# Performance work log

Hardware: AMD Instinct MI355X
Metric: run time of the kernel (lower is better)

The kernel has to match this reference:

```python
import jax, jax.numpy as jnp
import numpy as np

E = 512      # embed_size
H = 8        # heads
HD = E // H  # head_dim
TN = 288     # time_num
FE = 4       # forward_expansion
N, T = 64, 512


def layernorm(x, g, b, eps=1e-5):
    mu = jnp.mean(x, axis=-1, keepdims=True)
    var = jnp.mean((x - mu) ** 2, axis=-1, keepdims=True)
    return (x - mu) * jax.lax.rsqrt(var + eps) * g + b


def setup_inputs() -> dict:
    key = jax.random.key(0)
    ks = jax.random.split(key, 12)
    w = lambda k, sh: jax.random.normal(k, sh, dtype=jnp.float32) * 0.02
    return {
        "value": jax.random.normal(ks[0], (N, T, E), dtype=jnp.float32),
        "key_in": jax.random.normal(ks[1], (N, T, E), dtype=jnp.float32),
        "query": jax.random.normal(ks[2], (N, T, E), dtype=jnp.float32),
        "i": 37,
        # One_hot_encoder params: learned identity-init table + linear to embed
        "I_mat": jnp.eye(TN, dtype=jnp.float32),
        "oh_W": w(ks[3], (TN, E)), "oh_b": jnp.zeros((E,), jnp.float32),
        # per-head projections (shared across heads, as in the torch module)
        "Wv": w(ks[4], (HD, HD)), "Wk": w(ks[5], (HD, HD)), "Wq": w(ks[6], (HD, HD)),
        "Wo": w(ks[7], (E, E)), "bo": jnp.zeros((E,), jnp.float32),
        "g1": jnp.ones((E,), jnp.float32), "b1": jnp.zeros((E,), jnp.float32),
        "g2": jnp.ones((E,), jnp.float32), "b2": jnp.zeros((E,), jnp.float32),
        "W1": w(ks[8], (E, FE * E)), "bf1": jnp.zeros((FE * E,), jnp.float32),
        "W2": w(ks[9], (FE * E, E)), "bf2": jnp.zeros((E,), jnp.float32),
    }


def reference(value, key_in, query, i, I_mat, oh_W, oh_b, Wv, Wk, Wq, Wo, bo,
              g1, b1, g2, b2, W1, bf1, W2, bf2):
    n, t, c = query.shape
    # One_hot_encoder: rows i..i+T-1 (mod time_num) of learned table -> linear
    rows = (i + jnp.arange(t)) % TN
    onehot = I_mat[rows] @ oh_W + oh_b            # (T, E), broadcast over N
    q_in = query + onehot[None, :, :]
    # per-head projections
    v = value.reshape(n, t, H, HD) @ Wv           # (N,T,H,HD)
    k = key_in.reshape(n, t, H, HD) @ Wk
    qh = q_in.reshape(n, t, H, HD) @ Wq
    # attention (note: scale uses sqrt(embed_size), per original code)
    energy = jnp.einsum("nqhd,nkhd->nhqk", qh, k) / jnp.sqrt(jnp.float32(E))
    attn = jax.nn.softmax(energy, axis=-1)
    out = jnp.einsum("nhqk,nkhd->nqhd", attn, v).reshape(n, t, E)
    out = out @ Wo + bo
    # residual + LN + FFN + residual + LN (dropout=0 -> identity)
    x = layernorm(out + q_in, g1, b1)
    ff = jax.nn.relu(x @ W1 + bf1) @ W2 + bf2
    return layernorm(ff + x, g2, b2)
```

## Files before the change

### kernel.cpp

```cpp
#include <hip/hip_runtime.h>

typedef __attribute__((ext_vector_type(8))) short s16x8;
typedef __attribute__((ext_vector_type(4))) float f32x4;

#define TN 288

__device__ __forceinline__ unsigned short f2bf(float f) {
  union { float f; unsigned u; } v; v.f = f;
  unsigned r = v.u + 0x7fffu + ((v.u >> 16) & 1u);
  return (unsigned short)(r >> 16);
}
__device__ __forceinline__ float bf2f(unsigned short u) {
  union { float f; unsigned u; } v; v.u = ((unsigned)u) << 16;
  return v.f;
}
__device__ __forceinline__ unsigned lds_addr(const void* p) {
  return (unsigned)(unsigned long long)(const __attribute__((address_space(3))) char*)p;
}
__device__ __forceinline__ void async_copy16(unsigned short* lds, const unsigned short* g) {
  __builtin_amdgcn_global_load_lds(
      (const __attribute__((address_space(1))) unsigned int*)g,
      (__attribute__((address_space(3))) unsigned int*)lds, 16, 0, 0);
}

__device__ __forceinline__ void pack_body(const float* __restrict__ W,
    unsigned short* __restrict__ out, int N, long t) {
  int lr = (int)(t & 15);
  int lg = (int)((t >> 4) & 3);
  long g6 = t >> 6;
  int nt = N >> 4;
  int n16 = (int)(g6 % nt);
  int kb = (int)(g6 / nt) << 5;
  int k = kb + lg * 8;
  int col = n16 * 16 + lr;
  s16x8 v;
#pragma unroll
  for (int j = 0; j < 8; ++j) v[j] = (short)f2bf(W[(size_t)(k + j) * N + col]);
  *(s16x8*)(out + t * 8) = v;
}

__global__ __launch_bounds__(256) void prep_kernel(const int* __restrict__ pi,
    const float* __restrict__ I_mat, const float* __restrict__ ohW,
    const float* __restrict__ ohb, float* __restrict__ onehot,
    const float* __restrict__ Wv, const float* __restrict__ Wk,
    const float* __restrict__ Wq, unsigned short* __restrict__ Wv_b,
    unsigned short* __restrict__ Wk_b, unsigned short* __restrict__ Wq_b,
    const float* __restrict__ Wo, const float* __restrict__ W1,
    const float* __restrict__ W2, unsigned short* __restrict__ Wop,
    unsigned short* __restrict__ W1p, unsigned short* __restrict__ W2p) {
  int b = blockIdx.x, tid = threadIdx.x;
  if (b < 512) {
    int t = b;
    int r = (pi[0] + t) % TN;
    float acc0 = ohb[tid], acc1 = ohb[tid + 256];
    const float* Ir = I_mat + (size_t)r * TN;
    for (int j = 0; j < TN; ++j) {
      float iv = Ir[j];
      acc0 += iv * ohW[(size_t)j * 512 + tid];
      acc1 += iv * ohW[(size_t)j * 512 + tid + 256];
    }
    onehot[(size_t)t * 512 + tid] = acc0;
    onehot[(size_t)t * 512 + tid + 256] = acc1;
  } else if (b < 640) {
    pack_body(Wo, Wop, 512, (long)(b - 512) * 256 + tid);
  } else if (b < 1152) {
    pack_body(W1, W1p, 2048, (long)(b - 640) * 256 + tid);
  } else if (b < 1664) {
    pack_body(W2, W2p, 512, (long)(b - 1152) * 256 + tid);
  } else {
    int which = b - 1664;
    const float* src = which == 0 ? Wv : (which == 1 ? Wk : Wq);
    unsigned short* dst = which == 0 ? Wv_b : (which == 1 ? Wk_b : Wq_b);
    float sc = which == 2 ? 0.06375871424f : 1.f;
#pragma unroll
    for (int j = 0; j < 4; ++j) {
      int i = tid * 16 + j * 4;
      float4 f = *(const float4*)(src + i);
      unsigned lo = (unsigned)f2bf(f.x * sc) | ((unsigned)f2bf(f.y * sc) << 16);
      unsigned hi = (unsigned)f2bf(f.z * sc) | ((unsigned)f2bf(f.w * sc) << 16);
      *(uint2*)(dst + i) = make_uint2(lo, hi);
    }
  }
}

template<bool QIN, int OUTMODE>
__global__ __launch_bounds__(256) void proj_gemm(const float* __restrict__ A,
    const unsigned short* __restrict__ B, const float* __restrict__ onehot,
    unsigned short* __restrict__ C, int M, int N, int K) {
  __shared__ unsigned short As[64][40];
  __shared__ unsigned short Bs[64][40];
  __shared__ unsigned short Cs[64][72];
  const int m0 = blockIdx.x * 64, n0 = blockIdx.y * 64;
  const int tid = threadIdx.x, w = tid >> 6, l = tid & 63, lr = l & 15, lg = l >> 4;
  const int wr = (w >> 1) * 32, wc = (w & 1) * 32;
  const int aRow = (tid * 8) >> 5, aK = (tid * 8) & 31;
  const int bK = (tid * 8) >> 6, bCol = (tid * 8) & 63;
  f32x4 acc[2][2] = {};
  for (int kb = 0; kb < K; kb += 32) {
    size_t fl = (size_t)(m0 + aRow) * K + kb + aK;
    float4 f0 = *(const float4*)(A + fl);
    float4 f1 = *(const float4*)(A + fl + 4);
    if (QIN) {
      const float* oh = onehot + (fl & 262143);
      float4 o0 = *(const float4*)(oh);
      float4 o1 = *(const float4*)(oh + 4);
      f0.x += o0.x; f0.y += o0.y; f0.z += o0.z; f0.w += o0.w;
      f1.x += o1.x; f1.y += o1.y; f1.z += o1.z; f1.w += o1.w;
    }
    s16x8 av;
    av[0] = (short)f2bf(f0.x); av[1] = (short)f2bf(f0.y);
    av[2] = (short)f2bf(f0.z); av[3] = (short)f2bf(f0.w);
    av[4] = (short)f2bf(f1.x); av[5] = (short)f2bf(f1.y);
    av[6] = (short)f2bf(f1.z); av[7] = (short)f2bf(f1.w);
    *(s16x8*)&As[aRow][aK] = av;
    s16x8 bv = *(const s16x8*)(B + (size_t)(kb + bK) * N + n0 + bCol);
#pragma unroll
    for (int j = 0; j < 8; ++j) Bs[bCol + j][bK] = (unsigned short)bv[j];
    __syncthreads();
    s16x8 af0 = *(const s16x8*)&As[wr + lr][lg * 8];
    s16x8 af1 = *(const s16x8*)&As[wr + 16 + lr][lg * 8];
    s16x8 bf0 = *(const s16x8*)&Bs[wc + lr][lg * 8];
    s16x8 bf1 = *(const s16x8*)&Bs[wc + 16 + lr][lg * 8];
    acc[0][0] = __builtin_amdgcn_mfma_f32_16x16x32_bf16(af0, bf0, acc[0][0], 0, 0, 0);
    acc[0][1] = __builtin_amdgcn_mfma_f32_16x16x32_bf16(af0, bf1, acc[0][1], 0, 0, 0);
    acc[1][0] = __builtin_amdgcn_mfma_f32_16x16x32_bf16(af1, bf0, acc[1][0], 0, 0, 0);
    acc[1][1] = __builtin_amdgcn_mfma_f32_16x16x32_bf16(af1, bf1, acc[1][1], 0, 0, 0);
    __syncthreads();
  }
  if (OUTMODE == 0) {
#pragma unroll
    for (int fi = 0; fi < 2; ++fi)
#pragma unroll
      for (int fj = 0; fj < 2; ++fj)
#pragma unroll
        for (int r = 0; r < 4; ++r) {
          int row = m0 + wr + fi * 16 + lg * 4 + r;
          int col = n0 + wc + fj * 16 + lr;
          C[(size_t)row * N + col] = f2bf(acc[fi][fj][r]);
        }
  } else {
#pragma unroll
    for (int fi = 0; fi < 2; ++fi)
#pragma unroll
      for (int fj = 0; fj < 2; ++fj)
#pragma unroll
        for (int r = 0; r < 4; ++r)
          Cs[wr + fi * 16 + lg * 4 + r][wc + fj * 16 + lr] = f2bf(acc[fi][fj][r]);
    __syncthreads();
    int nIdx = m0 >> 12, t0 = (m0 >> 3) & 511;
#pragma unroll
    for (int it = 0; it < 2; ++it) {
      int p = tid + it * 256;
      int hh = p >> 6, d = p & 63;
      s16x8 vv;
#pragma unroll
      for (int j = 0; j < 8; ++j) vv[j] = (short)Cs[j * 8 + hh][d];
      *(s16x8*)(C + (((size_t)(nIdx * 8 + hh) * 64 + d) << 9) + t0) = vv;
    }
  }
}

template<bool RELU, bool OUTBF>
__global__ __launch_bounds__(256) void gemmF(
    const unsigned short* __restrict__ A, int lda,
    const unsigned short* __restrict__ Bp, int ldbp, int nOff,
    const float* __restrict__ bias, void* __restrict__ Cout, int ldc,
    int M, int K, int nby) {
  __shared__ unsigned short As[2][8192];
  const int tid = threadIdx.x, w = tid >> 6, l = tid & 63, lr = l & 15, lg = l >> 4;
  const int nwg = gridDim.x;
  const int bid = (blockIdx.x & 7) * (nwg >> 3) + (blockIdx.x >> 3);
  const int bx = bid / nby, by = bid % nby;
  const int m0 = bx * 128;
  const int wr = (w >> 1) * 64, wc = (w & 1) * 64;
  const int srow = tid >> 3, sc8 = tid & 7;
  const int gcol = (sc8 ^ (srow & 7)) * 8;
  const unsigned short* Ag = A + (size_t)(m0 + srow) * lda + gcol;
  const size_t ldaa = (size_t)32 * lda;
  const unsigned short* Bg = Bp +
      ((size_t)(nOff >> 4) + by * 8 + (wc >> 4)) * 512 + lg * 128 + lr * 8;
  const size_t bks = (size_t)ldbp * 512;

  f32x4 acc[4][4] = {};
  s16x8 b0[4], b1[4];

#pragma unroll
  for (int it = 0; it < 4; ++it)
    async_copy16(&As[0][(it * 256 + tid) * 8], Ag + it * ldaa);
#pragma unroll
  for (int fj = 0; fj < 4; ++fj) {
    b0[fj] = *(const s16x8*)(Bg + fj * 512);
    b1[fj] = *(const s16x8*)(Bg + bks + fj * 512);
  }
  __syncthreads();

  int buf = 0;
  for (int kb = 0; kb < K; kb += 64) {
    int kn = (kb + 64 < K) ? kb + 64 : 0;
#pragma unroll
    for (int it = 0; it < 4; ++it)
      async_copy16(&As[buf ^ 1][(it * 256 + tid) * 8], Ag + kn + it * ldaa);
    s16x8 b0n[4];
    {
      const unsigned short* p = Bg + ((size_t)(kn >> 5)) * bks;
#pragma unroll
      for (int fj = 0; fj < 4; ++fj) b0n[fj] = *(const s16x8*)(p + fj * 512);
    }
    {
      s16x8 af[4];
#pragma unroll
      for (int fi = 0; fi < 4; ++fi) {
        int row = wr + fi * 16 + lr;
        af[fi] = *(const s16x8*)&As[buf][row * 64 + ((lg ^ (row & 7)) * 8)];
      }
#pragma unroll
      for (int fi = 0; fi < 4; ++fi)
#pragma unroll
        for (int fj = 0; fj < 4; ++fj)
          acc[fi][fj] = __builtin_amdgcn_mfma_f32_16x16x32_bf16(af[fi], b0[fj], acc[fi][fj], 0, 0, 0);
    }
    s16x8 b1n[4];
    {
      const unsigned short* p = Bg + ((size_t)((kn + 32) >> 5)) * bks;
#pragma unroll
      for (int fj = 0; fj < 4; ++fj) b1n[fj] = *(const s16x8*)(p + fj * 512);
    }
    {
      s16x8 af[4];
#pragma unroll
      for (int fi = 0; fi < 4; ++fi) {
        int row = wr + fi * 16 + lr;
        af[fi] = *(const s16x8*)&As[buf][row * 64 + (((4 + lg) ^ (row & 7)) * 8)];
      }
#pragma unroll
      for (int fi = 0; fi < 4; ++fi)
#pragma unroll
        for (int fj = 0; fj < 4; ++fj)
          acc[fi][fj] = __builtin_amdgcn_mfma_f32_16x16x32_bf16(af[fi], b1[fj], acc[fi][fj], 0, 0, 0);
    }
    __syncthreads();
#pragma unroll
    for (int fj = 0; fj < 4; ++fj) { b0[fj] = b0n[fj]; b1[fj] = b1n[fj]; }
    buf ^= 1;
  }

#pragma unroll
  for (int fj = 0; fj < 4; ++fj) {
    int colL = by * 128 + wc + fj * 16 + lr;
    float bv = bias[nOff + colL];
#pragma unroll
    for (int fi = 0; fi < 4; ++fi)
#pragma unroll
      for (int r = 0; r < 4; ++r) {
        int row = m0 + wr + fi * 16 + lg * 4 + r;
        size_t ci = (size_t)row * ldc + colL;
        float v = acc[fi][fj][r] + bv;
        if (RELU) v = fmaxf(v, 0.f);
        if (OUTBF) ((unsigned short*)Cout)[ci] = f2bf(v);
        else ((float*)Cout)[ci] = v;
      }
  }
}

__global__ __launch_bounds__(256, 2) void attn_kernel(
    const unsigned short* __restrict__ Qp, const unsigned short* __restrict__ Kp,
    const unsigned short* __restrict__ Vt, unsigned short* __restrict__ Out) {
  __shared__ unsigned short KS[2][8192];
  __shared__ unsigned short P[4][16][132];
  const int bid = blockIdx.x;
  const int qh = bid >> 9, g = bid & 511, h = g & 7, n = g >> 3;
  const int tid = threadIdx.x, w = tid >> 6, l = tid & 63, lr = l & 15, lg = l >> 4;
  const int q0 = qh * 256;

  s16x8 qf[4][2];
#pragma unroll
  for (int rt = 0; rt < 4; ++rt) {
    const size_t qb = (((size_t)(n * 512 + q0 + w * 64 + rt * 16 + lr)) * 8 + h) * 64;
    qf[rt][0] = *(const s16x8*)(Qp + qb + lg * 8);
    qf[rt][1] = *(const s16x8*)(Qp + qb + 32 + lg * 8);
  }
  const unsigned short* Vb = Vt + ((size_t)(n * 8 + h)) * 32768 + (size_t)lr * 512 + lg * 8;

  const int krr = tid >> 3, kc8 = tid & 7;
  const int kcol = (kc8 ^ (krr & 7)) * 8;

  f32x4 oacc[4][4] = {};
  float m[4][4], lsum[4][4];
#pragma unroll
  for (int rt = 0; rt < 4; ++rt)
#pragma unroll
    for (int r = 0; r < 4; ++r) { m[rt][r] = -1e30f; lsum[rt][r] = 0.f; }
  s16x8 vreg[16];

#pragma unroll
  for (int it = 0; it < 4; ++it)
    async_copy16(&KS[0][(it * 256 + tid) * 8],
                 Kp + (((size_t)(n * 512 + it * 32 + krr)) * 8 + h) * 64 + kcol);
  __syncthreads();

#pragma unroll
  for (int c = 0; c < 4; ++c) {
    const int buf = c & 1;
    if (c < 3) {
#pragma unroll
      for (int it = 0; it < 4; ++it)
        async_copy16(&KS[buf ^ 1][(it * 256 + tid) * 8],
                     Kp + (((size_t)(n * 512 + (c + 1) * 128 + it * 32 + krr)) * 8 + h) * 64 + kcol);
    }
#pragma unroll
    for (int ks = 0; ks < 4; ++ks)
#pragma unroll
      for (int fj = 0; fj < 4; ++fj)
        vreg[ks * 4 + fj] = *(const s16x8*)(Vb + fj * 8192 + c * 128 + ks * 32);

#pragma unroll
    for (int rt = 0; rt < 4; ++rt) {
      f32x4 sacc[8];
      __builtin_amdgcn_s_setprio(1);
#pragma unroll
      for (int f = 0; f < 8; ++f) {
        int row = f * 16 + lr;
        s16x8 bk0 = *(const s16x8*)&KS[buf][row * 64 + ((lg ^ (row & 7)) * 8)];
        s16x8 bk1 = *(const s16x8*)&KS[buf][row * 64 + (((4 + lg) ^ (row & 7)) * 8)];
        f32x4 a = {};
        a = __builtin_amdgcn_mfma_f32_16x16x32_bf16(qf[rt][0], bk0, a, 0, 0, 0);
        a = __builtin_amdgcn_mfma_f32_16x16x32_bf16(qf[rt][1], bk1, a, 0, 0, 0);
        sacc[f] = a;
      }
      __builtin_amdgcn_s_setprio(0);

      float fs[4];
#pragma unroll
      for (int r = 0; r < 4; ++r) {
        float cm = sacc[0][r];
#pragma unroll
        for (int f = 1; f < 8; ++f) cm = fmaxf(cm, sacc[f][r]);
#pragma unroll
        for (int mk = 1; mk < 16; mk <<= 1) cm = fmaxf(cm, __shfl_xor(cm, mk));
        float mn = fmaxf(m[rt][r], cm);
        fs[r] = __builtin_amdgcn_exp2f(m[rt][r] - mn);
        m[rt][r] = mn;
        unsigned pa = lds_addr(&P[w][lg * 4 + r][lr]);
        float cs = 0.f;
#pragma unroll
        for (int f = 0; f < 8; ++f) {
          float p = __builtin_amdgcn_exp2f(sacc[f][r] - mn);
          asm volatile("ds_write_b16_d16_hi %0, %1 offset:%2"
                       :: "v"(pa), "v"(p), "i"(f * 32) : "memory");
          cs += p;
        }
#pragma unroll
        for (int mk = 1; mk < 16; mk <<= 1) cs += __shfl_xor(cs, mk);
        lsum[rt][r] = lsum[rt][r] * fs[r] + cs;
      }
#pragma unroll
      for (int fj = 0; fj < 4; ++fj)
#pragma unroll
        for (int r = 0; r < 4; ++r) oacc[rt][fj][r] *= fs[r];

      asm volatile("s_waitcnt lgkmcnt(0)" ::: "memory");
      __builtin_amdgcn_sched_barrier(0);
      __builtin_amdgcn_s_setprio(1);
#pragma unroll
      for (int ks = 0; ks < 4; ++ks) {
        s16x8 pa = *(const s16x8*)&P[w][lr][ks * 32 + lg * 8];
#pragma unroll
        for (int fj = 0; fj < 4; ++fj)
          oacc[rt][fj] = __builtin_amdgcn_mfma_f32_16x16x32_bf16(pa, vreg[ks * 4 + fj], oacc[rt][fj], 0, 0, 0);
      }
      __builtin_amdgcn_s_setprio(0);
    }
    __syncthreads();
  }

#pragma unroll
  for (int rt = 0; rt < 4; ++rt)
#pragma unroll
    for (int fj = 0; fj < 4; ++fj)
#pragma unroll
      for (int r = 0; r < 4; ++r) {
        int qrow = q0 + w * 64 + rt * 16 + lg * 4 + r;
        Out[((size_t)(n * 512 + qrow)) * 512 + h * 64 + fj * 16 + lr] =
            f2bf(oacc[rt][fj][r] / lsum[rt][r]);
      }
}

template<bool XBF, bool RBF, bool QIN, bool OUTBF>
__global__ __launch_bounds__(256) void ln_kernel(const void* __restrict__ Xv,
    const void* __restrict__ Rv, const float* __restrict__ onehot,
    const float* __restrict__ g, const float* __restrict__ bb,
    void* __restrict__ outv) {
  int row = blockIdx.x * 4 + (threadIdx.x >> 6);
  int l = threadIdx.x & 63;
  size_t base = (size_t)row * 512 + l * 8;
  float v[8];
  if (XBF) {
    s16x8 xv = *(const s16x8*)((const unsigned short*)Xv + base);
#pragma unroll
    for (int j = 0; j < 8; ++j) v[j] = bf2f((unsigned short)xv[j]);
  } else {
    const float* X = (const float*)Xv;
    float4 x0 = *(const float4*)(X + base);
    float4 x1 = *(const float4*)(X + base + 4);
    v[0] = x0.x; v[1] = x0.y; v[2] = x0.z; v[3] = x0.w;
    v[4] = x1.x; v[5] = x1.y; v[6] = x1.z; v[7] = x1.w;
  }
  if (RBF) {
    s16x8 rv = *(const s16x8*)((const unsigned short*)Rv + base);
#pragma unroll
    for (int j = 0; j < 8; ++j) v[j] += bf2f((unsigned short)rv[j]);
  } else {
    const float* R = (const float*)Rv;
    float4 r0 = *(const float4*)(R + base);
    float4 r1 = *(const float4*)(R + base + 4);
    v[0] += r0.x; v[1] += r0.y; v[2] += r0.z; v[3] += r0.w;
    v[4] += r1.x; v[5] += r1.y; v[6] += r1.z; v[7] += r1.w;
  }
  if (QIN) {
    size_t ob = (size_t)(row & 511) * 512 + l * 8;
    float4 o0 = *(const float4*)(onehot + ob);
    float4 o1 = *(const float4*)(onehot + ob + 4);
    v[0] += o0.x; v[1] += o0.y; v[2] += o0.z; v[3] += o0.w;
    v[4] += o1.x; v[5] += o1.y; v[6] += o1.z; v[7] += o1.w;
  }
  float s = 0.f, ss = 0.f;
#pragma unroll
  for (int j = 0; j < 8; ++j) { s += v[j]; ss += v[j] * v[j]; }
#pragma unroll
  for (int mk = 1; mk < 64; mk <<= 1) { s += __shfl_xor(s, mk); ss += __shfl_xor(ss, mk); }
  float mu = s * (1.f / 512.f);
  float inv = rsqrtf(ss * (1.f / 512.f) - mu * mu + 1e-5f);
#pragma unroll
  for (int j = 0; j < 8; ++j) {
    int e = l * 8 + j;
    float y = (v[j] - mu) * inv * g[e] + bb[e];
    if (OUTBF) ((unsigned short*)outv)[base + j] = f2bf(y);
    else ((float*)outv)[base + j] = y;
  }
}

extern "C" void kernel_launch(void* const* d_in, const int* in_sizes, int n_in,
                              void* d_out, int out_size, void* d_ws, size_t ws_size,
                              hipStream_t stream) {
  const float* value  = (const float*)d_in[0];
  const float* key_in = (const float*)d_in[1];
  const float* query  = (const float*)d_in[2];
  const int*   pi     = (const int*)d_in[3];
  const float* I_mat  = (const float*)d_in[4];
  const float* ohW    = (const float*)d_in[5];
  const float* ohb    = (const float*)d_in[6];
  const float* Wv     = (const float*)d_in[7];
  const float* Wk     = (const float*)d_in[8];
  const float* Wq     = (const float*)d_in[9];
  const float* Wo     = (const float*)d_in[10];
  const float* bo     = (const float*)d_in[11];
  const float* g1     = (const float*)d_in[12];
  const float* b1     = (const float*)d_in[13];
  const float* g2     = (const float*)d_in[14];
  const float* b2     = (const float*)d_in[15];
  const float* W1     = (const float*)d_in[16];
  const float* bf1    = (const float*)d_in[17];
  const float* W2     = (const float*)d_in[18];
  const float* bf2    = (const float*)d_in[19];

  char* ws = (char*)d_ws;
  const size_t MB = 1024 * 1024;
  unsigned short* q_p  = (unsigned short*)d_out;
  unsigned short* k_p  = q_p + 16777216;
  unsigned short* vT     = (unsigned short*)(ws + 0);
  unsigned short* attn_o = (unsigned short*)(ws + 32 * MB);
  unsigned short* x_b    = (unsigned short*)(ws + 64 * MB);
  unsigned short* ff1h   = (unsigned short*)(ws + 0);
  float*          onehot = (float*)(ws + 96 * MB);
  unsigned short* Wv_b   = (unsigned short*)(ws + 97 * MB);
  unsigned short* Wk_b   = Wv_b + 4096;
  unsigned short* Wq_b   = Wk_b + 4096;
  unsigned short* Wop    = Wq_b + 4096;
  unsigned short* W1p    = Wop + 262144;
  unsigned short* W2p    = W1p + 1048576;

  prep_kernel<<<1667, 256, 0, stream>>>(pi, I_mat, ohW, ohb, onehot,
      Wv, Wk, Wq, Wv_b, Wk_b, Wq_b, Wo, W1, W2, Wop, W1p, W2p);

  dim3 gp(4096, 1);
  proj_gemm<false, 1><<<gp, 256, 0, stream>>>(value,  Wv_b, nullptr, vT,  262144, 64, 64);
  proj_gemm<false, 0><<<gp, 256, 0, stream>>>(key_in, Wk_b, nullptr, k_p, 262144, 64, 64);
  proj_gemm<true,  0><<<gp, 256, 0, stream>>>(query,  Wq_b, onehot,  q_p, 262144, 64, 64);

  attn_kernel<<<1024, 256, 0, stream>>>(q_p, k_p, vT, attn_o);

  gemmF<false, true><<<1024, 256, 0, stream>>>(
      attn_o, 512, Wop, 32, 0, bo, x_b, 512, 32768, 512, 4);
  ln_kernel<true, false, true, true><<<8192, 256, 0, stream>>>(x_b, query, onehot, g1, b1, x_b);

  for (int hf = 0; hf < 2; ++hf) {
    const unsigned short* xh = x_b + (size_t)hf * 16384 * 512;
    gemmF<true, true><<<2048, 256, 0, stream>>>(
        xh, 512, W1p, 128, 0, bf1, ff1h, 2048, 16384, 512, 16);
    gemmF<false, false><<<512, 256, 0, stream>>>(
        ff1h, 2048, W2p, 32, 0, bf2, (float*)d_out + (size_t)hf * 16384 * 512, 512, 16384, 2048, 4);
  }
  ln_kernel<false, true, false, false><<<8192, 256, 0, stream>>>(d_out, x_b, nullptr, g2, b2, d_out);
}
```

Measured before the change: 510.9 us.

## Replace double-buffered async K loads with single padded LDS buffer in attention

The attention kernel drops the double-buffered async global-to-LDS K prefetch with XOR swizzle. It now uses a single padded (72-column) K tile filled by synchronous register loads, with barriers around each chunk load and the outer chunk loop no longer unrolled. This cuts LDS use and likely register pressure, but the K load is no longer overlapped with compute and the loop needs an extra barrier per chunk.

```diff
diff --git a/kernel.cpp b/kernel.cpp
--- a/kernel.cpp
+++ b/kernel.cpp
@@ -265,7 +265,7 @@
 __global__ __launch_bounds__(256, 2) void attn_kernel(
     const unsigned short* __restrict__ Qp, const unsigned short* __restrict__ Kp,
     const unsigned short* __restrict__ Vt, unsigned short* __restrict__ Out) {
-  __shared__ unsigned short KS[2][8192];
+  __shared__ unsigned short KS[128][72];
   __shared__ unsigned short P[4][16][132];
   const int bid = blockIdx.x;
   const int qh = bid >> 9, g = bid & 511, h = g & 7, n = g >> 3;
@@ -281,9 +281,6 @@
   }
   const unsigned short* Vb = Vt + ((size_t)(n * 8 + h)) * 32768 + (size_t)lr * 512 + lg * 8;
 
-  const int krr = tid >> 3, kc8 = tid & 7;
-  const int kcol = (kc8 ^ (krr & 7)) * 8;
-
   f32x4 oacc[4][4] = {};
   float m[4][4], lsum[4][4];
 #pragma unroll
@@ -293,38 +290,47 @@
   s16x8 vreg[16];
 
 #pragma unroll
-  for (int it = 0; it < 4; ++it)
-    async_copy16(&KS[0][(it * 256 + tid) * 8],
-                 Kp + (((size_t)(n * 512 + it * 32 + krr)) * 8 + h) * 64 + kcol);
+  for (int it = 0; it < 4; ++it) {
+    int idx = tid + it * 256;
+    int rr = idx >> 3, dd = (idx & 7) * 8;
+    *(s16x8*)&KS[rr][dd] =
+        *(const s16x8*)(Kp + (((size_t)(n * 512 + rr)) * 8 + h) * 64 + dd);
+  }
+#pragma unroll
+  for (int ks = 0; ks < 4; ++ks)
+#pragma unroll
+    for (int fj = 0; fj < 4; ++fj)
+      vreg[ks * 4 + fj] = *(const s16x8*)(Vb + fj * 8192 + ks * 32);
   __syncthreads();
 
-#pragma unroll
   for (int c = 0; c < 4; ++c) {
-    const int buf = c & 1;
-    if (c < 3) {
-#pragma unroll
-      for (int it = 0; it < 4; ++it)
-        async_copy16(&KS[buf ^ 1][(it * 256 + tid) * 8],
-                     Kp + (((size_t)(n * 512 + (c + 1) * 128 + it * 32 + krr)) * 8 + h) * 64 + kcol);
-    }
-#pragma unroll
-    for (int ks = 0; ks < 4; ++ks)
-#pragma unroll
-      for (int fj = 0; fj < 4; ++fj)
-        vreg[ks * 4 + fj] = *(const s16x8*)(Vb + fj * 8192 + c * 128 + ks * 32);
-
+    if (c) {
+      __syncthreads();
+#pragma unroll
+      for (int it = 0; it < 4; ++it) {
+        int idx = tid + it * 256;
+        int rr = idx >> 3, dd = (idx & 7) * 8;
+        *(s16x8*)&KS[rr][dd] =
+            *(const s16x8*)(Kp + (((size_t)(n * 512 + c * 128 + rr)) * 8 + h) * 64 + dd);
+      }
+#pragma unroll
+      for (int ks = 0; ks < 4; ++ks)
+#pragma unroll
+        for (int fj = 0; fj < 4; ++fj)
+          vreg[ks * 4 + fj] = *(const s16x8*)(Vb + fj * 8192 + c * 128 + ks * 32);
+      __syncthreads();
+    }
 #pragma unroll
     for (int rt = 0; rt < 4; ++rt) {
       f32x4 sacc[8];
       __builtin_amdgcn_s_setprio(1);
 #pragma unroll
       for (int f = 0; f < 8; ++f) {
-        int row = f * 16 + lr;
-        s16x8 bk0 = *(const s16x8*)&KS[buf][row * 64 + ((lg ^ (row & 7)) * 8)];
-        s16x8 bk1 = *(const s16x8*)&KS[buf][row * 64 + (((4 + lg) ^ (row & 7)) * 8)];
+        s16x8 b0 = *(const s16x8*)&KS[f * 16 + lr][lg * 8];
+        s16x8 b1 = *(const s16x8*)&KS[f * 16 + lr][32 + lg * 8];
         f32x4 a = {};
-        a = __builtin_amdgcn_mfma_f32_16x16x32_bf16(qf[rt][0], bk0, a, 0, 0, 0);
-        a = __builtin_amdgcn_mfma_f32_16x16x32_bf16(qf[rt][1], bk1, a, 0, 0, 0);
+        a = __builtin_amdgcn_mfma_f32_16x16x32_bf16(qf[rt][0], b0, a, 0, 0, 0);
+        a = __builtin_amdgcn_mfma_f32_16x16x32_bf16(qf[rt][1], b1, a, 0, 0, 0);
         sacc[f] = a;
       }
       __builtin_amdgcn_s_setprio(0);
@@ -370,7 +376,6 @@
       }
       __builtin_amdgcn_s_setprio(0);
     }
-    __syncthreads();
   }
 
 #pragma unroll
```

Result: faster. 468.3 us (-8.3%).
